# Kernel tuning notes

Measured on AMD Instinct MI355X. Metric: run time of the kernel, lower is better.

The kernel has to match this reference:

```python
import jax, jax.numpy as jnp
import numpy as np

B, L, D, DF, E = 8, 2048, 256, 1024, 1


def _layer_norm(x, g, b):
    mu = jnp.mean(x, axis=-1, keepdims=True)
    var = jnp.mean((x - mu) ** 2, axis=-1, keepdims=True)
    return (x - mu) * jax.lax.rsqrt(var + 1e-5) * g + b


def _ema_scan(z, a):
    # diagonal linear SSM: h_t = a*h_{t-1} + (1-a)*z_t, scanned over seq axis
    def step(h, zt):
        h = a * h + (1.0 - a) * zt
        return h, h
    zT = jnp.swapaxes(z, 0, 1)  # [L,B,D]
    h0 = jnp.zeros((z.shape[0], z.shape[2]), z.dtype)
    _, hs = jax.lax.scan(step, h0, zT)
    return jnp.swapaxes(hs, 0, 1)


def _mamba_block(x, m, Win, a_logit, Wout):
    zg = (x * m) @ Win                      # [B,L,2D]
    z, g = jnp.split(zg, 2, axis=-1)
    h = _ema_scan(z, jax.nn.sigmoid(a_logit))
    return ((h * jax.nn.silu(g)) @ Wout) * m


def _graph_agg(x, m, A_list, We):
    out = jnp.zeros_like(x)
    for e in range(We.shape[0]):
        A = A_list[e]
        agg = jnp.einsum('bij,bjd->bid', A, x * m)  # neighbor aggregation
        deg = jnp.clip(jnp.sum(A, axis=-1, keepdims=True), 1.0, None)
        out = out + (agg / deg) @ We[e]
    return jax.nn.relu(out) * m


def _masked_gather(x, idx, vc):
    # emulate: x_out[b,:vc] = x[b, idx[b,:vc]]; x_out[b,vc:] = x[b,vc:]
    pos = jnp.arange(x.shape[1])[None, :]
    im = jnp.where(pos < vc, idx, pos)
    return jnp.take_along_axis(x, im[:, :, None], axis=1)


def _forward(node_embedding, adjacency, gm1_Win, gm1_a_logit, gm1_Wout, gm2_We,
             gm_Win, gm_a_logit, gm_Wout, gm_We, ln1_g, ln1_b, ln2_g, ln2_b,
             ffn_W1, ffn_b1, ffn_W2, ffn_b2, Wv, bv,
             node_mask, sorted_list, reverse_list):
    X = node_embedding
    m = node_mask[:, :, None].astype(X.dtype)
    vc = jnp.sum(node_mask, axis=1, keepdims=True)  # [B,1] valid counts
    A_list = [adjacency]
    outs = []
    for si, ri in zip(sorted_list, reverse_list):
        se = _masked_gather(X, si, vc)
        bo = _mamba_block(se, m, gm1_Win, gm1_a_logit, gm1_Wout)
        re = _masked_gather(bo, ri, vc)
        outs.append(_graph_agg(re, m, A_list, gm2_We))
    outs.append(_mamba_block(X, m, gm_Win, gm_a_logit, gm_Wout) +
                _graph_agg(X, m, A_list, gm_We))
    # stack(dim=-1) + permute(0,1,3,2) + reshape == concat along feature dim
    Y = jnp.concatenate(outs, axis=-1) @ Wv + bv
    X1 = X + _layer_norm(Y, ln1_g, ln1_b)        # AddNorm, pre_ln, eval (no dropout)
    Y2 = jax.nn.relu(X1 @ ffn_W1 + ffn_b1) @ ffn_W2 + ffn_b2
    return X1 + _layer_norm(Y2, ln2_g, ln2_b)


def setup_inputs() -> dict:
    key = jax.random.key(0)
    ks = jax.random.split(key, 20)
    X = jax.random.normal(ks[0], (B, L, D), jnp.float32)
    lengths = jax.random.randint(ks[1], (B,), L // 2, L + 1)
    pos = jnp.arange(L)[None, :]
    M = (pos < lengths[:, None]).astype(jnp.int32)
    A = (jax.random.uniform(ks[2], (B, L, L)) < 0.004).astype(jnp.float32)
    A = A * M[:, :, None].astype(jnp.float32) * M[:, None, :].astype(jnp.float32)
    inp = {'node_embedding': X, 'node_mask': M, 'adjacency': A}
    for i in range(3):
        u = jax.random.uniform(ks[3 + i], (B, L))
        u = jnp.where(pos < lengths[:, None], u, 2.0 + pos.astype(jnp.float32))
        si = jnp.argsort(u, axis=1).astype(jnp.int32)   # perm of [0,vc) in prefix
        ri = jnp.argsort(si, axis=1).astype(jnp.int32)  # inverse permutation
        inp['sorted_indices_%d' % i] = si
        inp['reverse_indices_%d' % i] = ri
    def w(k, shape):
        return 0.02 * jax.random.normal(k, shape, jnp.float32)
    inp.update(
        gm1_Win=w(ks[6], (D, 2 * D)), gm1_a_logit=w(ks[7], (D,)), gm1_Wout=w(ks[8], (D, D)),
        gm2_We=w(ks[9], (E, D, D)),
        gm_Win=w(ks[10], (D, 2 * D)), gm_a_logit=w(ks[11], (D,)), gm_Wout=w(ks[12], (D, D)),
        gm_We=w(ks[13], (E, D, D)),
        ln1_g=jnp.ones((D,), jnp.float32), ln1_b=jnp.zeros((D,), jnp.float32),
        ln2_g=jnp.ones((D,), jnp.float32), ln2_b=jnp.zeros((D,), jnp.float32),
        ffn_W1=w(ks[14], (D, DF)), ffn_b1=jnp.zeros((DF,), jnp.float32),
        ffn_W2=w(ks[15], (DF, D)), ffn_b2=jnp.zeros((D,), jnp.float32),
        Wv=w(ks[16], (4 * D, D)), bv=jnp.zeros((D,), jnp.float32),
    )
    return inp


def reference(node_embedding, node_mask, adjacency,
              sorted_indices_0, sorted_indices_1, sorted_indices_2,
              reverse_indices_0, reverse_indices_1, reverse_indices_2,
              gm1_Win, gm1_a_logit, gm1_Wout, gm2_We,
              gm_Win, gm_a_logit, gm_Wout, gm_We,
              ln1_g, ln1_b, ln2_g, ln2_b,
              ffn_W1, ffn_b1, ffn_W2, ffn_b2, Wv, bv):
    return _forward(node_embedding, adjacency, gm1_Win, gm1_a_logit, gm1_Wout, gm2_We,
                    gm_Win, gm_a_logit, gm_Wout, gm_We, ln1_g, ln1_b, ln2_g, ln2_b,
                    ffn_W1, ffn_b1, ffn_W2, ffn_b2, Wv, bv,
                    node_mask,
                    [sorted_indices_0, sorted_indices_1, sorted_indices_2],
                    [reverse_indices_0, reverse_indices_1, reverse_indices_2])
```

## Files before the change

### kernel.cpp

```cpp
#include <hip/hip_runtime.h>

typedef unsigned short u16;
typedef unsigned int u32;
typedef unsigned long long u64;

#define BB 8
#define LL 2048
#define DD 256
#define NB (BB * LL)
#define NBR 4
#define NRT (NBR * NB)
#define NCH 32
#define CHL (LL / NCH)
#define CAP 64

typedef __attribute__((ext_vector_type(8))) __bf16 bf16x8;
typedef __attribute__((ext_vector_type(4))) float f32x4;

__device__ __forceinline__ float b2f(u16 u) {
    union { u32 u; float f; } x; x.u = ((u32)u) << 16; return x.f;
}
__device__ __forceinline__ u16 f2b(float f) {
    union { float f; u32 u; } x; x.f = f;
    u32 r = (x.u >> 16) & 1u;
    x.u += 0x7FFFu + r;
    return (u16)(x.u >> 16);
}
__device__ __forceinline__ float sigm(float x) { return 1.f / (1.f + __expf(-x)); }

#define GLD(gp, lp) __builtin_amdgcn_global_load_lds( \
    (const __attribute__((address_space(1))) void*)(gp), \
    (__attribute__((address_space(3))) void*)(lp), 16, 0, 0)

__global__ void xb_kernel(const float* __restrict__ X, const int* __restrict__ maskp,
                          u16* __restrict__ Xb) {
    int g = blockIdx.x * 256 + threadIdx.x;
    int r = g >> 6;
    float4 v = maskp[r] ? *(const float4*)(X + (size_t)g * 4)
                        : (float4){0.f, 0.f, 0.f, 0.f};
    union { u64 q; u16 h[4]; } pk;
    pk.h[0] = f2b(v.x); pk.h[1] = f2b(v.y); pk.h[2] = f2b(v.z); pk.h[3] = f2b(v.w);
    *(u64*)(Xb + (size_t)g * 4) = pk.q;
}

struct TrArgs {
    const float* s[9];
    u16* d[9];
    int K[9], N[9], tr[9];
    int beg[10];
};
__global__ void transpose_all(TrArgs a) {
    int blk = blockIdx.x;
    int i = 0;
    while (blk >= a.beg[i + 1]) ++i;
    int idx = (blk - a.beg[i]) * 256 + threadIdx.x;
    int K = a.K[i], N = a.N[i];
    if (idx >= K * N) return;
    if (a.tr[i]) {
        int k = idx / N, n = idx - k * N;
        a.d[i][(size_t)n * K + k] = f2b(a.s[i][idx]);
    } else {
        a.d[i][idx] = f2b(a.s[i][idx]);
    }
}

__global__ void csr_kernel(const float* __restrict__ Adj,
                           const int* __restrict__ ri0, const int* __restrict__ ri1,
                           const int* __restrict__ ri2,
                           int* __restrict__ csr4, int* __restrict__ cnt,
                           float* __restrict__ deg) {
    int w = threadIdx.x >> 6, lane = threadIdx.x & 63;
    int row = blockIdx.x * 4 + w;
    int rowb = row & ~(LL - 1);
    const float* arow = Adj + (size_t)row * LL;
    int base = 0;
    for (int c = 0; c < LL / 256; ++c) {
        float4 v = *(const float4*)(arow + c * 256 + lane * 4);
#pragma unroll
        for (int e = 0; e < 4; ++e) {
            float f = (e == 0) ? v.x : (e == 1) ? v.y : (e == 2) ? v.z : v.w;
            bool nz = (f != 0.f);
            u64 m = __ballot(nz);
            if (nz) {
                int pos = base + __popcll(m & ((1ull << lane) - 1ull));
                if (pos < CAP) {
                    int j = c * 256 + lane * 4 + e;
                    csr4[((size_t)(3 * NB + row)) * CAP + pos] = j;
                    csr4[((size_t)(0 * NB + row)) * CAP + pos] = ri0[rowb + j];
                    csr4[((size_t)(1 * NB + row)) * CAP + pos] = ri1[rowb + j];
                    csr4[((size_t)(2 * NB + row)) * CAP + pos] = ri2[rowb + j];
                }
            }
            base += __popcll(m);
        }
    }
    if (lane == 0) {
        cnt[row] = base < CAP ? base : CAP;
        deg[row] = (float)(base < 1 ? 1 : base);
    }
}

__global__ __launch_bounds__(256)
void gemm_win_kernel(const u16* __restrict__ Xb,
                     const int* __restrict__ si0, const int* __restrict__ si1,
                     const int* __restrict__ si2,
                     const u16* __restrict__ Bt1, const u16* __restrict__ Bt2,
                     u16* __restrict__ zbuf, u16* __restrict__ gbuf)
{
    __shared__ __align__(16) u16 As[2][128 * 32];
    __shared__ __align__(16) u16 Bs[2][128 * 32];
    int tid = threadIdx.x, lane = tid & 63;
    int w = tid >> 6, wm = w >> 1, wn = w & 1;
    int rowBase = blockIdx.x * 128, colBase = blockIdx.y * 128;
    const u16* Bt = (rowBase < 3 * NB) ? Bt1 : Bt2;

    const u16* pa[2];
    const u16* pb[2];
#pragma unroll
    for (int rep = 0; rep < 2; ++rep) {
        int s = rep * 256 + tid;
        int row = s >> 2, kk = (s & 3) << 3;
        int rg = rowBase + row;
        int br = rg >> 14, r = rg & (NB - 1), b = r >> 11, l = r & (LL - 1);
        int src = (br == 0) ? si0[r] : (br == 1) ? si1[r] : (br == 2) ? si2[r] : l;
        pa[rep] = Xb + ((size_t)(b << 11) + src) * DD + kk;
        pb[rep] = Bt + (size_t)(colBase + row) * 256 + kk;
    }

    f32x4 acc[4][4];
#pragma unroll
    for (int m = 0; m < 4; ++m)
#pragma unroll
        for (int n = 0; n < 4; ++n) acc[m][n] = (f32x4){0.f, 0.f, 0.f, 0.f};

#pragma unroll
    for (int rep = 0; rep < 2; ++rep) {
        int s = rep * 256 + tid;
        GLD(pa[rep], As[0] + s * 8);
        GLD(pb[rep], Bs[0] + s * 8);
    }
    int p = 0;
    for (int t = 0; t < 8; ++t) {
        if (t + 1 < 8) {
            int k0 = (t + 1) * 32;
#pragma unroll
            for (int rep = 0; rep < 2; ++rep) {
                int s = rep * 256 + tid;
                GLD(pa[rep] + k0, As[p ^ 1] + s * 8);
                GLD(pb[rep] + k0, Bs[p ^ 1] + s * 8);
            }
            asm volatile("s_waitcnt vmcnt(4)" ::: "memory");
        } else {
            asm volatile("s_waitcnt vmcnt(0)" ::: "memory");
        }
        __builtin_amdgcn_s_barrier();
        int kq = (lane >> 4) << 3;
        bf16x8 av[4], bw[4];
#pragma unroll
        for (int m = 0; m < 4; ++m)
            av[m] = *(const bf16x8*)(As[p] + (wm * 64 + m * 16 + (lane & 15)) * 32 + kq);
#pragma unroll
        for (int n = 0; n < 4; ++n)
            bw[n] = *(const bf16x8*)(Bs[p] + (wn * 64 + n * 16 + (lane & 15)) * 32 + kq);
#pragma unroll
        for (int m = 0; m < 4; ++m)
#pragma unroll
            for (int n = 0; n < 4; ++n)
                acc[m][n] = __builtin_amdgcn_mfma_f32_16x16x32_bf16(av[m], bw[n], acc[m][n], 0, 0, 0);
        __builtin_amdgcn_s_barrier();
        p ^= 1;
    }

    u16* Cz;
    int cb;
    if (colBase < 256) { Cz = zbuf; cb = colBase; }
    else               { Cz = gbuf; cb = colBase - 256; }
    int cBase = cb + wn * 64 + (lane & 15);
    int rBase = rowBase + wm * 64 + ((lane >> 4) << 2);
#pragma unroll
    for (int m = 0; m < 4; ++m)
#pragma unroll
        for (int n = 0; n < 4; ++n)
#pragma unroll
            for (int r = 0; r < 4; ++r)
                Cz[(size_t)(rBase + m * 16 + r) * 256 + (cBase + n * 16)] = f2b(acc[m][n][r]);
}

__global__ __launch_bounds__(256)
void gemm_kernel(const u16* __restrict__ A1, const u16* __restrict__ A2, int asplit,
                 const u16* __restrict__ Bt1, const u16* __restrict__ Bt2,
                 const u16* __restrict__ Bt3, int split1, int split2,
                 void* __restrict__ Cout, const float* __restrict__ bias,
                 int N, int K, int mode)
{
    __shared__ __align__(16) u16 As[2][128 * 32];
    __shared__ __align__(16) u16 Bs[2][128 * 32];
    int tid = threadIdx.x;
    int lane = tid & 63;
    int w = tid >> 6, wm = w >> 1, wn = w & 1;
    int rowBase = blockIdx.x * 128, colBase = blockIdx.y * 128;
    const u16* Bt = (rowBase < split1) ? Bt1 : (rowBase < split2) ? Bt2 : Bt3;
    const u16* Arow = (rowBase < asplit) ? A1 + (size_t)rowBase * K
                                         : A2 + (size_t)(rowBase - asplit) * K;

    const u16* pa[2];
    const u16* pb[2];
#pragma unroll
    for (int rep = 0; rep < 2; ++rep) {
        int s = rep * 256 + tid;
        int row = s >> 2, kk = (s & 3) << 3;
        pa[rep] = Arow + (size_t)row * K + kk;
        pb[rep] = Bt + (size_t)(colBase + row) * K + kk;
    }

    f32x4 acc[4][4];
#pragma unroll
    for (int m = 0; m < 4; ++m)
#pragma unroll
        for (int n = 0; n < 4; ++n) acc[m][n] = (f32x4){0.f, 0.f, 0.f, 0.f};

    int nt = K >> 5;
#pragma unroll
    for (int rep = 0; rep < 2; ++rep) {
        int s = rep * 256 + tid;
        GLD(pa[rep], As[0] + s * 8);
        GLD(pb[rep], Bs[0] + s * 8);
    }
    int p = 0;
    for (int t = 0; t < nt; ++t) {
        if (t + 1 < nt) {
            int k0 = (t + 1) << 5;
#pragma unroll
            for (int rep = 0; rep < 2; ++rep) {
                int s = rep * 256 + tid;
                GLD(pa[rep] + k0, As[p ^ 1] + s * 8);
                GLD(pb[rep] + k0, Bs[p ^ 1] + s * 8);
            }
            asm volatile("s_waitcnt vmcnt(4)" ::: "memory");
        } else {
            asm volatile("s_waitcnt vmcnt(0)" ::: "memory");
        }
        __builtin_amdgcn_s_barrier();
        int kq = (lane >> 4) << 3;
        bf16x8 av[4], bw[4];
#pragma unroll
        for (int m = 0; m < 4; ++m)
            av[m] = *(const bf16x8*)(As[p] + (wm * 64 + m * 16 + (lane & 15)) * 32 + kq);
#pragma unroll
        for (int n = 0; n < 4; ++n)
            bw[n] = *(const bf16x8*)(Bs[p] + (wn * 64 + n * 16 + (lane & 15)) * 32 + kq);
#pragma unroll
        for (int m = 0; m < 4; ++m)
#pragma unroll
            for (int n = 0; n < 4; ++n)
                acc[m][n] = __builtin_amdgcn_mfma_f32_16x16x32_bf16(av[m], bw[n], acc[m][n], 0, 0, 0);
        __builtin_amdgcn_s_barrier();
        p ^= 1;
    }

    int cBase = colBase + wn * 64 + (lane & 15);
    int rBase = rowBase + wm * 64 + ((lane >> 4) << 2);
    if (mode == 0) {
        float* C = (float*)Cout;
#pragma unroll
        for (int m = 0; m < 4; ++m)
#pragma unroll
            for (int n = 0; n < 4; ++n)
#pragma unroll
                for (int r = 0; r < 4; ++r)
                    C[(size_t)(rBase + m * 16 + r) * N + (cBase + n * 16)] = acc[m][n][r];
    } else {
        u16* C = (u16*)Cout;
        float bz[4];
#pragma unroll
        for (int n = 0; n < 4; ++n) bz[n] = bias ? bias[cBase + n * 16] : 0.f;
#pragma unroll
        for (int m = 0; m < 4; ++m)
#pragma unroll
            for (int n = 0; n < 4; ++n)
#pragma unroll
                for (int r = 0; r < 4; ++r) {
                    float v = acc[m][n][r] + bz[n];
                    if (mode == 1) v = v > 0.f ? v : 0.f;
                    C[(size_t)(rBase + m * 16 + r) * N + (cBase + n * 16)] = f2b(v);
                }
    }
}

__global__ void scan_carry_kernel(const u16* __restrict__ z4, const float* __restrict__ alog1,
                                  const float* __restrict__ alog2, float* __restrict__ carry) {
    int bid = blockIdx.x;
    int br = bid >> 8, b = (bid >> 5) & 7, c = bid & 31;
    int d0 = threadIdx.x * 2;
    const float* al = (br < 3) ? alog1 : alog2;
    float aA = sigm(al[d0]), aB = sigm(al[d0 + 1]);
    float hA = 0.f, hB = 0.f;
    const u16* zp = z4 + ((size_t)(br * NB + b * LL + c * CHL) * DD) + d0;
    for (int t = 0; t < CHL; ++t) {
        u32 v = *(const u32*)(zp + (size_t)t * DD);
        hA = aA * hA + (1.f - aA) * b2f((u16)v);
        hB = aB * hB + (1.f - aB) * b2f((u16)(v >> 16));
    }
    carry[(size_t)bid * DD + d0] = hA;
    carry[(size_t)bid * DD + d0 + 1] = hB;
}

__global__ void scan_apply_kernel(const u16* __restrict__ z4, const u16* __restrict__ g4,
                                  const float* __restrict__ alog1, const float* __restrict__ alog2,
                                  const float* __restrict__ carry, u16* __restrict__ U4) {
    int bid = blockIdx.x;
    int br = bid >> 8, b = (bid >> 5) & 7, c = bid & 31;
    int d0 = threadIdx.x * 2;
    const float* al = (br < 3) ? alog1 : alog2;
    float aA = sigm(al[d0]), aB = sigm(al[d0 + 1]);
    float aPA = aA, aPB = aB;
#pragma unroll
    for (int i = 0; i < 6; ++i) { aPA *= aPA; aPB *= aPB; }
    float hA = 0.f, hB = 0.f;
    const float* cp = carry + ((size_t)((br * 8 + b) * 32)) * DD + d0;
    for (int cc = 0; cc < c; ++cc) {
        float2 cv = *(const float2*)(cp + (size_t)cc * DD);
        hA = cv.x + aPA * hA;
        hB = cv.y + aPB * hB;
    }
    size_t rowOff = ((size_t)(br * NB + b * LL + c * CHL)) * DD + d0;
    const u16* zp = z4 + rowOff;
    const u16* gp = g4 + rowOff;
    u16* up = U4 + rowOff;
    for (int t = 0; t < CHL; ++t) {
        u32 zv = *(const u32*)(zp + (size_t)t * DD);
        u32 gv = *(const u32*)(gp + (size_t)t * DD);
        float gA = b2f((u16)gv), gB = b2f((u16)(gv >> 16));
        hA = aA * hA + (1.f - aA) * b2f((u16)zv);
        hB = aB * hB + (1.f - aB) * b2f((u16)(zv >> 16));
        u32 o = (u32)f2b(hA * gA * sigm(gA)) | ((u32)f2b(hB * gB * sigm(gB)) << 16);
        *(u32*)(up + (size_t)t * DD) = o;
    }
}

__global__ void agg4_kernel(const u16* __restrict__ V5, const int* __restrict__ csr4,
                            const int* __restrict__ cnt, const float* __restrict__ deg,
                            const int* __restrict__ maskp, u16* __restrict__ Yin) {
    int tr = threadIdx.x & 31;
    int rsub = threadIdx.x >> 5;
    int rg = blockIdx.x * 8 + rsub;
    int br = rg >> 14, r = rg & (NB - 1), b = r >> 11;
    int n = cnt[r];
    const int* lst = csr4 + ((size_t)(br * NB + r)) * CAP;
    const u16* srcB = V5 + ((size_t)((br < 3 ? br : 4) * NB + (b << 11))) * DD + tr * 8;
    float acc[8] = {0.f, 0.f, 0.f, 0.f, 0.f, 0.f, 0.f, 0.f};
    int i = 0;
    for (; i + 4 <= n; i += 4) {
        int4 il = *(const int4*)(lst + i);
        union { uint4 q; u16 h[8]; } v0, v1, v2, v3;
        v0.q = *(const uint4*)(srcB + (size_t)il.x * DD);
        v1.q = *(const uint4*)(srcB + (size_t)il.y * DD);
        v2.q = *(const uint4*)(srcB + (size_t)il.z * DD);
        v3.q = *(const uint4*)(srcB + (size_t)il.w * DD);
#pragma unroll
        for (int k = 0; k < 8; ++k)
            acc[k] += b2f(v0.h[k]) + b2f(v1.h[k]) + b2f(v2.h[k]) + b2f(v3.h[k]);
    }
    for (; i < n; ++i) {
        int idx = lst[i];
        union { uint4 q; u16 h[8]; } v;
        v.q = *(const uint4*)(srcB + (size_t)idx * DD);
#pragma unroll
        for (int k = 0; k < 8; ++k) acc[k] += b2f(v.h[k]);
    }
    float inv = 1.f / deg[r];
    int msk = maskp[r];
    union { uint4 q; u16 h[8]; } mo;
    if (br == 3) mo.q = *(const uint4*)(V5 + ((size_t)(3 * NB + r)) * DD + tr * 8);
    union { uint4 q; u16 h[8]; } o;
#pragma unroll
    for (int k = 0; k < 8; ++k) {
        float v = acc[k] * inv;
        v = v > 0.f ? v : 0.f;
        if (br == 3) v += b2f(mo.h[k]);
        v = msk ? v : 0.f;
        o.h[k] = f2b(v);
    }
    *(uint4*)(Yin + (size_t)r * 1024 + (br << 8) + tr * 8) = o.q;
}

__global__ void ln1_kernel(const float* __restrict__ Yt, const float* __restrict__ bvp,
                           const float* __restrict__ X, const float* __restrict__ gp,
                           const float* __restrict__ bp, float* __restrict__ X1f,
                           u16* __restrict__ X1b) {
    int wv = threadIdx.x >> 6, lane = threadIdx.x & 63;
    int r = blockIdx.x * 4 + wv;
    int d0 = lane << 2;
    float4 yv = *(const float4*)(Yt + (size_t)r * DD + d0);
    float4 bb = *(const float4*)(bvp + d0);
    float x[4] = { yv.x + bb.x, yv.y + bb.y, yv.z + bb.z, yv.w + bb.w };
    float s = x[0] + x[1] + x[2] + x[3];
#pragma unroll
    for (int o = 32; o > 0; o >>= 1) s += __shfl_xor(s, o, 64);
    float mu = s * (1.f / DD);
    float dx[4], ss = 0.f;
#pragma unroll
    for (int k = 0; k < 4; ++k) { dx[k] = x[k] - mu; ss += dx[k] * dx[k]; }
#pragma unroll
    for (int o = 32; o > 0; o >>= 1) ss += __shfl_xor(ss, o, 64);
    float rstd = rsqrtf(ss * (1.f / DD) + 1e-5f);
    float4 g4 = *(const float4*)(gp + d0);
    float4 b4 = *(const float4*)(bp + d0);
    float4 xv = *(const float4*)(X + (size_t)r * DD + d0);
    float gg[4] = { g4.x, g4.y, g4.z, g4.w };
    float bz[4] = { b4.x, b4.y, b4.z, b4.w };
    float xx[4] = { xv.x, xv.y, xv.z, xv.w };
    float o4[4];
    union { u64 q; u16 h[4]; } pk;
#pragma unroll
    for (int k = 0; k < 4; ++k) {
        float y = dx[k] * rstd * gg[k] + bz[k];
        o4[k] = xx[k] + y;
        pk.h[k] = f2b(o4[k]);
    }
    *(float4*)(X1f + (size_t)r * DD + d0) = (float4){o4[0], o4[1], o4[2], o4[3]};
    *(u64*)(X1b + (size_t)r * DD + d0) = pk.q;
}

__global__ void ln2_kernel(const float* __restrict__ Y2, const float* __restrict__ b2p,
                           const float* __restrict__ X1f, const float* __restrict__ gp,
                           const float* __restrict__ bp, float* __restrict__ Out) {
    int wv = threadIdx.x >> 6, lane = threadIdx.x & 63;
    int r = blockIdx.x * 4 + wv;
    int d0 = lane << 2;
    float4 yv = *(const float4*)(Y2 + (size_t)r * DD + d0);
    float4 bb = *(const float4*)(b2p + d0);
    float x[4] = { yv.x + bb.x, yv.y + bb.y, yv.z + bb.z, yv.w + bb.w };
    float s = x[0] + x[1] + x[2] + x[3];
#pragma unroll
    for (int o = 32; o > 0; o >>= 1) s += __shfl_xor(s, o, 64);
    float mu = s * (1.f / DD);
    float dx[4], ss = 0.f;
#pragma unroll
    for (int k = 0; k < 4; ++k) { dx[k] = x[k] - mu; ss += dx[k] * dx[k]; }
#pragma unroll
    for (int o = 32; o > 0; o >>= 1) ss += __shfl_xor(ss, o, 64);
    float rstd = rsqrtf(ss * (1.f / DD) + 1e-5f);
    float4 g4 = *(const float4*)(gp + d0);
    float4 b4 = *(const float4*)(bp + d0);
    float4 xv = *(const float4*)(X1f + (size_t)r * DD + d0);
    float o4[4];
    o4[0] = xv.x + dx[0] * rstd * g4.x + b4.x;
    o4[1] = xv.y + dx[1] * rstd * g4.y + b4.y;
    o4[2] = xv.z + dx[2] * rstd * g4.z + b4.z;
    o4[3] = xv.w + dx[3] * rstd * g4.w + b4.w;
    *(float4*)(Out + (size_t)r * DD + d0) = (float4){o4[0], o4[1], o4[2], o4[3]};
}

extern "C" void kernel_launch(void* const* d_in, const int* in_sizes, int n_in,
                              void* d_out, int out_size, void* d_ws, size_t ws_size,
                              hipStream_t stream) {
    const float* X      = (const float*)d_in[0];
    const int* maskp    = (const int*)d_in[1];
    const float* Adj    = (const float*)d_in[2];
    const int* si[3]    = { (const int*)d_in[3], (const int*)d_in[5], (const int*)d_in[7] };
    const int* ri[3]    = { (const int*)d_in[4], (const int*)d_in[6], (const int*)d_in[8] };
    const float* gm1_Win  = (const float*)d_in[9];
    const float* gm1_alog = (const float*)d_in[10];
    const float* gm1_Wout = (const float*)d_in[11];
    const float* gm2_We   = (const float*)d_in[12];
    const float* gm_Win   = (const float*)d_in[13];
    const float* gm_alog  = (const float*)d_in[14];
    const float* gm_Wout  = (const float*)d_in[15];
    const float* gm_We    = (const float*)d_in[16];
    const float* ln1_g    = (const float*)d_in[17];
    const float* ln1_b    = (const float*)d_in[18];
    const float* ln2_g    = (const float*)d_in[19];
    const float* ln2_b    = (const float*)d_in[20];
    const float* ffn_W1   = (const float*)d_in[21];
    const float* ffn_b1   = (const float*)d_in[22];
    const float* ffn_W2   = (const float*)d_in[23];
    const float* ffn_b2   = (const float*)d_in[24];
    const float* Wv       = (const float*)d_in[25];
    const float* bv       = (const float*)d_in[26];
    float* Out = (float*)d_out;

    char* ws = (char*)d_ws;
    size_t off = 0;
    auto alloc = [&](size_t bytes) { size_t o = off; off += (bytes + 255) & ~(size_t)255; return o; };

    u16* WinT1  = (u16*)(ws + alloc((size_t)512 * 256 * 2));
    u16* WinT   = (u16*)(ws + alloc((size_t)512 * 256 * 2));
    u16* WoutT  = (u16*)(ws + alloc((size_t)256 * 256 * 2));
    u16* WeT1   = (u16*)(ws + alloc((size_t)256 * 256 * 2));
    u16* WeT    = (u16*)(ws + alloc((size_t)256 * 256 * 2));
    u16* WvT    = (u16*)(ws + alloc((size_t)256 * 1024 * 2));
    u16* W1T    = (u16*)(ws + alloc((size_t)1024 * 256 * 2));
    u16* W2T    = (u16*)(ws + alloc((size_t)256 * 1024 * 2));
    u16* WoutL  = (u16*)(ws + alloc((size_t)256 * 256 * 2));
    u16* Wc1T   = (u16*)(ws + alloc((size_t)256 * 256 * 2));
    u16* Xb     = (u16*)(ws + alloc((size_t)NB * DD * 2));
    int* csr4 = (int*)(ws + alloc((size_t)4 * NB * CAP * 4));
    int* cnt = (int*)(ws + alloc((size_t)NB * 4));
    float* deg = (float*)(ws + alloc((size_t)NB * 4));
    float* carry = (float*)(ws + alloc((size_t)NBR * BB * NCH * DD * 4));
    u16* zbuf = (u16*)(ws + alloc((size_t)NRT * DD * 2));
    u16* gbuf = (u16*)(ws + alloc((size_t)NRT * DD * 2));
    u16* U4   = (u16*)(ws + alloc((size_t)4 * NB * DD * 2));
    u16* V5   = (u16*)(ws + alloc((size_t)5 * NB * DD * 2));
    u16* Yin  = (u16*)(ws + alloc((size_t)NB * 1024 * 2));
    float* tmpY  = (float*)(ws + alloc((size_t)NB * DD * 4));
    float* X1f   = (float*)(ws + alloc((size_t)NB * DD * 4));
    u16* X1b     = (u16*)(ws + alloc((size_t)NB * DD * 2));
    u16* H       = (u16*)(ws + alloc((size_t)NB * 1024 * 2));
    float* tmpY2 = (float*)(ws + alloc((size_t)NB * DD * 4));
    (void)ws_size; (void)in_sizes; (void)n_in; (void)out_size;

    xb_kernel<<<NB * DD / 4 / 256, 256, 0, stream>>>(X, maskp, Xb);

    TrArgs ta;
    const float* srcs[9] = { gm1_Win, gm_Win, gm_Wout, gm2_We, gm_We, Wv, ffn_W1, ffn_W2, gm1_Wout };
    u16* dsts[9]         = { WinT1,   WinT,   WoutT,   WeT1,   WeT,   WvT, W1T,   W2T,    WoutL };
    int Ks[9] = { 256, 256, 256, 256, 256, 1024, 256, 1024, 256 };
    int Ns[9] = { 512, 512, 256, 256, 256, 256, 1024, 256, 256 };
    int trs[9] = { 1, 1, 1, 1, 1, 1, 1, 1, 0 };
    int cum = 0;
    for (int i = 0; i < 9; ++i) {
        ta.s[i] = srcs[i]; ta.d[i] = dsts[i]; ta.K[i] = Ks[i]; ta.N[i] = Ns[i]; ta.tr[i] = trs[i];
        ta.beg[i] = cum; cum += (Ks[i] * Ns[i]) / 256;
    }
    ta.beg[9] = cum;
    transpose_all<<<cum, 256, 0, stream>>>(ta);

    gemm_kernel<<<dim3(2, 2), 256, 0, stream>>>(
        WeT1, WeT1, 1 << 30, WoutL, WoutL, WoutL, 1 << 30, 1 << 30,
        (void*)Wc1T, nullptr, 256, 256, 2);

    csr_kernel<<<NB / 4, 256, 0, stream>>>(Adj, ri[0], ri[1], ri[2], csr4, cnt, deg);

    gemm_win_kernel<<<dim3(NRT / 128, 512 / 128), 256, 0, stream>>>(
        Xb, si[0], si[1], si[2], WinT1, WinT, zbuf, gbuf);

    scan_carry_kernel<<<NBR * BB * NCH, 128, 0, stream>>>(zbuf, gm1_alog, gm_alog, carry);
    scan_apply_kernel<<<NBR * BB * NCH, 128, 0, stream>>>(zbuf, gbuf, gm1_alog, gm_alog, carry, U4);

    gemm_kernel<<<dim3(5 * NB / 128, 2), 256, 0, stream>>>(
        U4, Xb, 4 * NB, Wc1T, WoutT, WeT, 3 * NB, 4 * NB,
        (void*)V5, nullptr, 256, 256, 2);

    agg4_kernel<<<NRT / 8, 256, 0, stream>>>(V5, csr4, cnt, deg, maskp, Yin);

    gemm_kernel<<<dim3(NB / 128, 2), 256, 0, stream>>>(
        Yin, Yin, 1 << 30, WvT, WvT, WvT, 1 << 30, 1 << 30,
        (void*)tmpY, nullptr, 256, 1024, 0);

    ln1_kernel<<<NB / 4, 256, 0, stream>>>(tmpY, bv, X, ln1_g, ln1_b, X1f, X1b);

    gemm_kernel<<<dim3(NB / 128, 8), 256, 0, stream>>>(
        X1b, X1b, 1 << 30, W1T, W1T, W1T, 1 << 30, 1 << 30,
        (void*)H, ffn_b1, 1024, 256, 1);

    gemm_kernel<<<dim3(NB / 128, 2), 256, 0, stream>>>(
        H, H, 1 << 30, W2T, W2T, W2T, 1 << 30, 1 << 30,
        (void*)tmpY2, nullptr, 256, 1024, 0);

    ln2_kernel<<<NB / 4, 256, 0, stream>>>(tmpY2, ffn_b2, X1f, ln2_g, ln2_b, Out);
}
```

Measured before the change: 275.7 us.

## Split-K the two K=1024 projection GEMMs into bf16 partials summed in LayerNorm

The Wv and FFN-W2 GEMMs (N=256, K=1024) now use a new split-K-by-2 kernel. This doubles the grid from 256 to 512 blocks, and each half writes a bf16 partial result that the LayerNorm kernels add together with the bias. The fp32 intermediates are replaced by two bf16 buffers. The Xb conversion kernel is folded into the weight-transpose launch to save one launch. The trade-off is an extra bf16 rounding of each partial sum before the add, which costs some precision, plus an extra read in the LN kernels.

```diff
diff --git a/kernel.cpp b/kernel.cpp
--- a/kernel.cpp
+++ b/kernel.cpp
@@ -32,27 +32,29 @@
     (const __attribute__((address_space(1))) void*)(gp), \
     (__attribute__((address_space(3))) void*)(lp), 16, 0, 0)
 
-__global__ void xb_kernel(const float* __restrict__ X, const int* __restrict__ maskp,
-                          u16* __restrict__ Xb) {
-    int g = blockIdx.x * 256 + threadIdx.x;
-    int r = g >> 6;
-    float4 v = maskp[r] ? *(const float4*)(X + (size_t)g * 4)
-                        : (float4){0.f, 0.f, 0.f, 0.f};
-    union { u64 q; u16 h[4]; } pk;
-    pk.h[0] = f2b(v.x); pk.h[1] = f2b(v.y); pk.h[2] = f2b(v.z); pk.h[3] = f2b(v.w);
-    *(u64*)(Xb + (size_t)g * 4) = pk.q;
-}
-
 struct TrArgs {
     const float* s[9];
     u16* d[9];
     int K[9], N[9], tr[9];
-    int beg[10];
+    int beg[11];
+    const float* xsrc;
+    const int* maskp;
+    u16* xdst;
 };
 __global__ void transpose_all(TrArgs a) {
     int blk = blockIdx.x;
     int i = 0;
     while (blk >= a.beg[i + 1]) ++i;
+    if (i == 9) {
+        int g = (blk - a.beg[9]) * 256 + threadIdx.x;
+        int r = g >> 6;
+        float4 v = a.maskp[r] ? *(const float4*)(a.xsrc + (size_t)g * 4)
+                              : (float4){0.f, 0.f, 0.f, 0.f};
+        union { u64 q; u16 h[4]; } pk;
+        pk.h[0] = f2b(v.x); pk.h[1] = f2b(v.y); pk.h[2] = f2b(v.z); pk.h[3] = f2b(v.w);
+        *(u64*)(a.xdst + (size_t)g * 4) = pk.q;
+        return;
+    }
     int idx = (blk - a.beg[i]) * 256 + threadIdx.x;
     int K = a.K[i], N = a.N[i];
     if (idx >= K * N) return;
@@ -260,31 +262,98 @@
 
     int cBase = colBase + wn * 64 + (lane & 15);
     int rBase = rowBase + wm * 64 + ((lane >> 4) << 2);
-    if (mode == 0) {
-        float* C = (float*)Cout;
+    u16* C = (u16*)Cout;
+    float bz[4];
+#pragma unroll
+    for (int n = 0; n < 4; ++n) bz[n] = bias ? bias[cBase + n * 16] : 0.f;
+#pragma unroll
+    for (int m = 0; m < 4; ++m)
+#pragma unroll
+        for (int n = 0; n < 4; ++n)
+#pragma unroll
+            for (int r = 0; r < 4; ++r) {
+                float v = acc[m][n][r] + bz[n];
+                if (mode == 1) v = v > 0.f ? v : 0.f;
+                C[(size_t)(rBase + m * 16 + r) * N + (cBase + n * 16)] = f2b(v);
+            }
+}
+
+__global__ __launch_bounds__(256)
+void gemm_splitk2_kernel(const u16* __restrict__ A, const u16* __restrict__ Bt,
+                         u16* __restrict__ C0, u16* __restrict__ C1)
+{
+    __shared__ __align__(16) u16 As[2][128 * 32];
+    __shared__ __align__(16) u16 Bs[2][128 * 32];
+    int tid = threadIdx.x;
+    int lane = tid & 63;
+    int w = tid >> 6, wm = w >> 1, wn = w & 1;
+    int rowBase = blockIdx.x * 128, colBase = blockIdx.y * 128;
+    int koff = blockIdx.z * 512;
+
+    const u16* pa[2];
+    const u16* pb[2];
+#pragma unroll
+    for (int rep = 0; rep < 2; ++rep) {
+        int s = rep * 256 + tid;
+        int row = s >> 2, kk = (s & 3) << 3;
+        pa[rep] = A + (size_t)(rowBase + row) * 1024 + koff + kk;
+        pb[rep] = Bt + (size_t)(colBase + row) * 1024 + koff + kk;
+    }
+
+    f32x4 acc[4][4];
+#pragma unroll
+    for (int m = 0; m < 4; ++m)
+#pragma unroll
+        for (int n = 0; n < 4; ++n) acc[m][n] = (f32x4){0.f, 0.f, 0.f, 0.f};
+
+#pragma unroll
+    for (int rep = 0; rep < 2; ++rep) {
+        int s = rep * 256 + tid;
+        GLD(pa[rep], As[0] + s * 8);
+        GLD(pb[rep], Bs[0] + s * 8);
+    }
+    int p = 0;
+    for (int t = 0; t < 16; ++t) {
+        if (t + 1 < 16) {
+            int k0 = (t + 1) << 5;
+#pragma unroll
+            for (int rep = 0; rep < 2; ++rep) {
+                int s = rep * 256 + tid;
+                GLD(pa[rep] + k0, As[p ^ 1] + s * 8);
+                GLD(pb[rep] + k0, Bs[p ^ 1] + s * 8);
+            }
+            asm volatile("s_waitcnt vmcnt(4)" ::: "memory");
+        } else {
+            asm volatile("s_waitcnt vmcnt(0)" ::: "memory");
+        }
+        __builtin_amdgcn_s_barrier();
+        int kq = (lane >> 4) << 3;
+        bf16x8 av[4], bw[4];
 #pragma unroll
         for (int m = 0; m < 4; ++m)
+            av[m] = *(const bf16x8*)(As[p] + (wm * 64 + m * 16 + (lane & 15)) * 32 + kq);
+#pragma unroll
+        for (int n = 0; n < 4; ++n)
+            bw[n] = *(const bf16x8*)(Bs[p] + (wn * 64 + n * 16 + (lane & 15)) * 32 + kq);
+#pragma unroll
+        for (int m = 0; m < 4; ++m)
 #pragma unroll
             for (int n = 0; n < 4; ++n)
-#pragma unroll
-                for (int r = 0; r < 4; ++r)
-                    C[(size_t)(rBase + m * 16 + r) * N + (cBase + n * 16)] = acc[m][n][r];
-    } else {
-        u16* C = (u16*)Cout;
-        float bz[4];
-#pragma unroll
-        for (int n = 0; n < 4; ++n) bz[n] = bias ? bias[cBase + n * 16] : 0.f;
-#pragma unroll
-        for (int m = 0; m < 4; ++m)
-#pragma unroll
-            for (int n = 0; n < 4; ++n)
-#pragma unroll
-                for (int r = 0; r < 4; ++r) {
-                    float v = acc[m][n][r] + bz[n];
-                    if (mode == 1) v = v > 0.f ? v : 0.f;
-                    C[(size_t)(rBase + m * 16 + r) * N + (cBase + n * 16)] = f2b(v);
-                }
-    }
+                acc[m][n] = __builtin_amdgcn_mfma_f32_16x16x32_bf16(av[m], bw[n], acc[m][n], 0, 0, 0);
+        __builtin_amdgcn_s_barrier();
+        p ^= 1;
+    }
+
+    u16* C = blockIdx.z ? C1 : C0;
+    int cBase = colBase + wn * 64 + (lane & 15);
+    int rBase = rowBase + wm * 64 + ((lane >> 4) << 2);
+#pragma unroll
+    for (int m = 0; m < 4; ++m)
+#pragma unroll
+        for (int n = 0; n < 4; ++n)
+#pragma unroll
+            for (int r = 0; r < 4; ++r)
+                C[(size_t)(rBase + m * 16 + r) * 256 + (cBase + n * 16)] = f2b(acc[m][n][r]);
 }
 
 __global__ void scan_carry_kernel(const u16* __restrict__ z4, const float* __restrict__ alog1,
@@ -384,16 +453,21 @@
     *(uint4*)(Yin + (size_t)r * 1024 + (br << 8) + tr * 8) = o.q;
 }
 
-__global__ void ln1_kernel(const float* __restrict__ Yt, const float* __restrict__ bvp,
+__global__ void ln1_kernel(const u16* __restrict__ Ya, const u16* __restrict__ Yb,
+                           const float* __restrict__ bvp,
                            const float* __restrict__ X, const float* __restrict__ gp,
                            const float* __restrict__ bp, float* __restrict__ X1f,
                            u16* __restrict__ X1b) {
     int wv = threadIdx.x >> 6, lane = threadIdx.x & 63;
     int r = blockIdx.x * 4 + wv;
     int d0 = lane << 2;
-    float4 yv = *(const float4*)(Yt + (size_t)r * DD + d0);
+    union { u64 q; u16 h[4]; } ya, yb;
+    ya.q = *(const u64*)(Ya + (size_t)r * DD + d0);
+    yb.q = *(const u64*)(Yb + (size_t)r * DD + d0);
     float4 bb = *(const float4*)(bvp + d0);
-    float x[4] = { yv.x + bb.x, yv.y + bb.y, yv.z + bb.z, yv.w + bb.w };
+    float x[4];
+#pragma unroll
+    for (int k = 0; k < 4; ++k) x[k] = b2f(ya.h[k]) + b2f(yb.h[k]) + (&bb.x)[k];
     float s = x[0] + x[1] + x[2] + x[3];
 #pragma unroll
     for (int o = 32; o > 0; o >>= 1) s += __shfl_xor(s, o, 64);
@@ -407,30 +481,32 @@
     float4 g4 = *(const float4*)(gp + d0);
     float4 b4 = *(const float4*)(bp + d0);
     float4 xv = *(const float4*)(X + (size_t)r * DD + d0);
-    float gg[4] = { g4.x, g4.y, g4.z, g4.w };
-    float bz[4] = { b4.x, b4.y, b4.z, b4.w };
-    float xx[4] = { xv.x, xv.y, xv.z, xv.w };
     float o4[4];
     union { u64 q; u16 h[4]; } pk;
 #pragma unroll
     for (int k = 0; k < 4; ++k) {
-        float y = dx[k] * rstd * gg[k] + bz[k];
-        o4[k] = xx[k] + y;
+        float y = dx[k] * rstd * (&g4.x)[k] + (&b4.x)[k];
+        o4[k] = (&xv.x)[k] + y;
         pk.h[k] = f2b(o4[k]);
     }
     *(float4*)(X1f + (size_t)r * DD + d0) = (float4){o4[0], o4[1], o4[2], o4[3]};
     *(u64*)(X1b + (size_t)r * DD + d0) = pk.q;
 }
 
-__global__ void ln2_kernel(const float* __restrict__ Y2, const float* __restrict__ b2p,
+__global__ void ln2_kernel(const u16* __restrict__ Ya, const u16* __restrict__ Yb,
+                           const float* __restrict__ b2p,
                            const float* __restrict__ X1f, const float* __restrict__ gp,
                            const float* __restrict__ bp, float* __restrict__ Out) {
     int wv = threadIdx.x >> 6, lane = threadIdx.x & 63;
     int r = blockIdx.x * 4 + wv;
     int d0 = lane << 2;
-    float4 yv = *(const float4*)(Y2 + (size_t)r * DD + d0);
+    union { u64 q; u16 h[4]; } ya, yb;
+    ya.q = *(const u64*)(Ya + (size_t)r * DD + d0);
+    yb.q = *(const u64*)(Yb + (size_t)r * DD + d0);
     float4 bb = *(const float4*)(b2p + d0);
-    float x[4] = { yv.x + bb.x, yv.y + bb.y, yv.z + bb.z, yv.w + bb.w };
+    float x[4];
+#pragma unroll
+    for (int k = 0; k < 4; ++k) x[k] = b2f(ya.h[k]) + b2f(yb.h[k]) + (&bb.x)[k];
     float s = x[0] + x[1] + x[2] + x[3];
 #pragma unroll
     for (int o = 32; o > 0; o >>= 1) s += __shfl_xor(s, o, 64);
@@ -445,10 +521,9 @@
     float4 b4 = *(const float4*)(bp + d0);
     float4 xv = *(const float4*)(X1f + (size_t)r * DD + d0);
     float o4[4];
-    o4[0] = xv.x + dx[0] * rstd * g4.x + b4.x;
-    o4[1] = xv.y + dx[1] * rstd * g4.y + b4.y;
-    o4[2] = xv.z + dx[2] * rstd * g4.z + b4.z;
-    o4[3] = xv.w + dx[3] * rstd * g4.w + b4.w;
+#pragma unroll
+    for (int k = 0; k < 4; ++k)
+        o4[k] = (&xv.x)[k] + dx[k] * rstd * (&g4.x)[k] + (&b4.x)[k];
     *(float4*)(Out + (size_t)r * DD + d0) = (float4){o4[0], o4[1], o4[2], o4[3]};
 }
 
@@ -504,14 +579,14 @@
     u16* U4   = (u16*)(ws + alloc((size_t)4 * NB * DD * 2));
     u16* V5   = (u16*)(ws + alloc((size_t)5 * NB * DD * 2));
     u16* Yin  = (u16*)(ws + alloc((size_t)NB * 1024 * 2));
-    float* tmpY  = (float*)(ws + alloc((size_t)NB * DD * 4));
+    u16* tmpYa  = (u16*)(ws + alloc((size_t)NB * DD * 2));
+    u16* tmpYb  = (u16*)(ws + alloc((size_t)NB * DD * 2));
     float* X1f   = (float*)(ws + alloc((size_t)NB * DD * 4));
     u16* X1b     = (u16*)(ws + alloc((size_t)NB * DD * 2));
     u16* H       = (u16*)(ws + alloc((size_t)NB * 1024 * 2));
-    float* tmpY2 = (float*)(ws + alloc((size_t)NB * DD * 4));
+    u16* tmpY2a  = (u16*)(ws + alloc((size_t)NB * DD * 2));
+    u16* tmpY2b  = (u16*)(ws + alloc((size_t)NB * DD * 2));
     (void)ws_size; (void)in_sizes; (void)n_in; (void)out_size;
-
-    xb_kernel<<<NB * DD / 4 / 256, 256, 0, stream>>>(X, maskp, Xb);
 
     TrArgs ta;
     const float* srcs[9] = { gm1_Win, gm_Win, gm_Wout, gm2_We, gm_We, Wv, ffn_W1, ffn_W2, gm1_Wout };
@@ -524,7 +599,9 @@
         ta.s[i] = srcs[i]; ta.d[i] = dsts[i]; ta.K[i] = Ks[i]; ta.N[i] = Ns[i]; ta.tr[i] = trs[i];
         ta.beg[i] = cum; cum += (Ks[i] * Ns[i]) / 256;
     }
-    ta.beg[9] = cum;
+    ta.beg[9] = cum; cum += NB * DD / 4 / 256;
+    ta.beg[10] = cum;
+    ta.xsrc = X; ta.maskp = maskp; ta.xdst = Xb;
     transpose_all<<<cum, 256, 0, stream>>>(ta);
 
     gemm_kernel<<<dim3(2, 2), 256, 0, stream>>>(
@@ -545,19 +622,15 @@
 
     agg4_kernel<<<NRT / 8, 256, 0, stream>>>(V5, csr4, cnt, deg, maskp, Yin);
 
-    gemm_kernel<<<dim3(NB / 128, 2), 256, 0, stream>>>(
-        Yin, Yin, 1 << 30, WvT, WvT, WvT, 1 << 30, 1 << 30,
-        (void*)tmpY, nullptr, 256, 1024, 0);
-
-    ln1_kernel<<<NB / 4, 256, 0, stream>>>(tmpY, bv, X, ln1_g, ln1_b, X1f, X1b);
+    gemm_splitk2_kernel<<<dim3(NB / 128, 2, 2), 256, 0, stream>>>(Yin, WvT, tmpYa, tmpYb);
+
+    ln1_kernel<<<NB / 4, 256, 0, stream>>>(tmpYa, tmpYb, bv, X, ln1_g, ln1_b, X1f, X1b);
 
     gemm_kernel<<<dim3(NB / 128, 8), 256, 0, stream>>>(
         X1b, X1b, 1 << 30, W1T, W1T, W1T, 1 << 30, 1 << 30,
         (void*)H, ffn_b1, 1024, 256, 1);
 
-    gemm_kernel<<<dim3(NB / 128, 2), 256, 0, stream>>>(
-        H, H, 1 << 30, W2T, W2T, W2T, 1 << 30, 1 << 30,
-        (void*)tmpY2, nullptr, 256, 1024, 0);
-
-    ln2_kernel<<<NB / 4, 256, 0, stream>>>(tmpY2, ffn_b2, X1f, ln2_g, ln2_b, Out);
-}
+    gemm_splitk2_kernel<<<dim3(NB / 128, 2, 2), 256, 0, stream>>>(H, W2T, tmpY2a, tmpY2b);
+
+    ln2_kernel<<<NB / 4, 256, 0, stream>>>(tmpY2a, tmpY2b, ffn_b2, X1f, ln2_g, ln2_b, Out);
+}
```

Measured after the change: 257.5 us. -6.6%, faster.
